# Performance work log

Measured on AMD Instinct MI355X. Metric: run time of the kernel, lower is better.

Reference implementation:

```python
import jax, jax.numpy as jnp
import numpy as np

B, R, C, D = 4, 64, 64, 512   # batch, rows, cols, hidden_size
H, DH = 4, 128                # num_heads, channels per head
S = R * C                     # flattened attention length (raster order)
NEG = -1e6                    # mask value used by coltran


def setup_inputs():
    key = jax.random.key(0)
    ks = jax.random.split(key, 7)
    def w(k, shape, s=0.02):
        return jax.random.normal(k, shape, jnp.float32) * s
    return dict(
        x=jax.random.normal(ks[0], (B, R, C, D), jnp.float32),
        wq=w(ks[1], (D, H, DH)),
        wk=w(ks[2], (D, H, DH)),
        wv=w(ks[3], (D, H, DH)),
        wo=w(ks[4], (H, DH, D)),
        # relative_attention_bias_i: [num_heads, 2*length] per axis
        # (zero-init in the original; randomized here so the bias path is exercised)
        rel_row=w(ks[5], (H, 2 * R)),
        rel_col=w(ks[6], (H, 2 * C)),
    )


def _axis_bias(w, L):
    """att_utils.relative_attn_bias: [H, 2L] -> [H, Lq, Lk], b[h,q,k] = w[h, L-1 + k - q]."""
    pos = jnp.arange(L)
    idx = (L - 1) + pos[None, :] - pos[:, None]  # [Lq, Lk] in [0, 2L-2]
    return w[:, idx]


def reference(x, wq, wk, wv, wo, rel_row, rel_col):
    # q/k/v projections: contract channel axis into [H, DH]
    q = jnp.einsum('brcd,dhe->brche', x, wq) * (DH ** -0.5)
    k = jnp.einsum('brcd,dhe->brche', x, wk)
    v = jnp.einsum('brcd,dhe->brche', x, wv)
    q = q.reshape(B, S, H, DH)
    k = k.reshape(B, S, H, DH)
    v = v.reshape(B, S, H, DH)

    # factorized N-D relative attention bias -> [H, S, S]
    brow = _axis_bias(rel_row, R)  # [H, R, R]
    bcol = _axis_bias(rel_col, C)  # [H, C, C]
    bias = (brow[:, :, None, :, None] + bcol[:, None, :, None, :]).reshape(H, S, S)

    # 'future' mask in raster order: disallow k > q
    mask = jnp.triu(jnp.full((S, S), NEG, dtype=jnp.float32), 1)

    logits = jnp.einsum('bqhe,bkhe->bhqk', q, k) + bias[None] + mask[None, None]
    p = jax.nn.softmax(logits, axis=-1)
    o = jnp.einsum('bhqk,bkhe->bqhe', p, v)       # weighted sum over keys
    out = jnp.einsum('bqhe,hed->bqd', o, wo)      # final projection, contract_axes=2
    return out.reshape(B, R, C, D)
```

## Files before the change

### kernel.cpp

```cpp
#include <hip/hip_runtime.h>
#include <cstdint>

typedef unsigned short u16;
typedef __attribute__((ext_vector_type(8))) short short8;
typedef __attribute__((ext_vector_type(4))) short short4v;
typedef __attribute__((ext_vector_type(4))) float f32x4;
typedef __attribute__((ext_vector_type(4))) unsigned short u16x4;
typedef __attribute__((ext_vector_type(2))) float f32x2;
typedef __attribute__((ext_vector_type(2))) __bf16 bf16x2;


#if defined(__has_builtin)
#if __has_builtin(__builtin_amdgcn_mfma_f32_16x16x16bf16_1k)
#define HAVE_MFMA16 1
#endif
#endif

__device__ __forceinline__ uint32_t pk2(float a, float b) {
  f32x2 t;
  t[0] = a;
  t[1] = b;
  bf16x2 h = __builtin_convertvector(t, bf16x2);
  return __builtin_bit_cast(uint32_t, h);
}

__device__ __forceinline__ u16 f2b(float f) {
  return __builtin_bit_cast(u16, (__bf16)f);
}

__device__ __forceinline__ uint2 pkbf16x4(f32x4 v, float s) {
  uint2 r;
  r.x = pk2(v[0] * s, v[1] * s);
  r.y = pk2(v[2] * s, v[3] * s);
  return r;
}

__device__ __forceinline__ void dma16(const u16* g, u16* l) {
  __builtin_amdgcn_global_load_lds(
      (const __attribute__((address_space(1))) unsigned int*)(uintptr_t)g,
      (__attribute__((address_space(3))) unsigned int*)(uintptr_t)l, 16, 0, 0);
}

#define LDS_FENCE() asm volatile("s_waitcnt lgkmcnt(0)" ::: "memory")

__global__ __launch_bounds__(256) void xcast(const float* __restrict__ x,
                                             u16* __restrict__ xb) {
  const size_t i = (size_t)(blockIdx.x * 256 + threadIdx.x) * 8;
  const float4 a = *(const float4*)(x + i);
  const float4 b = *(const float4*)(x + i + 4);
  uint4 o;
  o.x = pk2(a.x, a.y);
  o.y = pk2(a.z, a.w);
  o.z = pk2(b.x, b.y);
  o.w = pk2(b.z, b.w);
  *(uint4*)(xb + i) = o;
}

__global__ __launch_bounds__(256) void transpose_all(const float* __restrict__ wq,
                                                     const float* __restrict__ wk,
                                                     const float* __restrict__ wv,
                                                     const float* __restrict__ wo,
                                                     u16* __restrict__ wT,
                                                     u16* __restrict__ woT) {
  __shared__ __align__(16) u16 T[64][68];
  const int mtx = blockIdx.y;
  const float* src = (mtx == 0) ? wq : (mtx == 1) ? wk : (mtx == 2) ? wv : wo;
  u16* dst = (mtx < 3) ? (wT + (size_t)mtx * 262144) : woT;
  const int tr = blockIdx.x >> 3, tc = blockIdx.x & 7;
  const int tid = threadIdx.x;
#pragma unroll
  for (int p = 0; p < 4; ++p) {
    int i = p * 256 + tid;
    int row = i >> 4, c4 = i & 15;
    float4 v = *(const float4*)(src + (size_t)(tr * 64 + row) * 512 + tc * 64 + c4 * 4);
    T[c4 * 4 + 0][row] = f2b(v.x);
    T[c4 * 4 + 1][row] = f2b(v.y);
    T[c4 * 4 + 2][row] = f2b(v.z);
    T[c4 * 4 + 3][row] = f2b(v.w);
  }
  __syncthreads();
#pragma unroll
  for (int p = 0; p < 4; ++p) {
    int i = p * 256 + tid;
    int row = i >> 4, c4 = i & 15;
    *(u16x4*)(dst + (size_t)(tc * 64 + row) * 512 + tr * 64 + c4 * 4) =
        *(const u16x4*)&T[row][c4 * 4];
  }
}

__global__ __launch_bounds__(512, 2) void qkv_gemm(const u16* __restrict__ xb,
                                                   const u16* __restrict__ wT_all,
                                                   u16* __restrict__ qbuf,
                                                   u16* __restrict__ kbuf,
                                                   u16* __restrict__ vtbuf) {
  __shared__ __align__(16) u16 smem[128 * 72 + 256 * 72];
  u16* As = smem;
  u16* Bs = smem + 128 * 72;
  const int tid = threadIdx.x;
  const int wave = tid >> 6, lane = tid & 63, quad = lane >> 4, l16 = lane & 15;
  const int wm = wave >> 2, wn = wave & 3;
  const int m0 = blockIdx.x * 128;
  const int which = blockIdx.y >> 1;
  const int n0 = (blockIdx.y & 1) * 256;
  const u16* wTb = wT_all + (size_t)which * 262144 + (size_t)n0 * 512;

  f32x4 acc[4][4];
  const f32x4 fz = {0.f, 0.f, 0.f, 0.f};
#pragma unroll
  for (int i = 0; i < 4; ++i)
#pragma unroll
    for (int j = 0; j < 4; ++j) acc[i][j] = fz;

  for (int k0 = 0; k0 < 512; k0 += 64) {
#pragma unroll
    for (int p = 0; p < 2; ++p) {
      int i = p * 512 + tid, row = i >> 3, c8 = i & 7;
      uint4 v = *(const uint4*)(xb + (size_t)(m0 + row) * 512 + k0 + c8 * 8);
      *(uint4*)&As[row * 72 + c8 * 8] = v;
    }
#pragma unroll
    for (int p = 0; p < 4; ++p) {
      int i = p * 512 + tid, row = i >> 3, c8 = i & 7;
      uint4 v = *(const uint4*)(wTb + (size_t)row * 512 + k0 + c8 * 8);
      *(uint4*)&Bs[row * 72 + c8 * 8] = v;
    }
    __syncthreads();
#pragma unroll
    for (int ks = 0; ks < 2; ++ks) {
      short8 xf[4], wf[4];
#pragma unroll
      for (int mt = 0; mt < 4; ++mt)
        xf[mt] = *(const short8*)&As[(wm * 64 + mt * 16 + l16) * 72 + ks * 32 + quad * 8];
#pragma unroll
      for (int nt = 0; nt < 4; ++nt)
        wf[nt] = *(const short8*)&Bs[(wn * 64 + nt * 16 + l16) * 72 + ks * 32 + quad * 8];
      if (which < 2) {
#pragma unroll
        for (int mt = 0; mt < 4; ++mt)
#pragma unroll
          for (int nt = 0; nt < 4; ++nt)
            acc[mt][nt] = __builtin_amdgcn_mfma_f32_16x16x32_bf16(wf[nt], xf[mt],
                                                                  acc[mt][nt], 0, 0, 0);
      } else {
#pragma unroll
        for (int mt = 0; mt < 4; ++mt)
#pragma unroll
          for (int nt = 0; nt < 4; ++nt)
            acc[mt][nt] = __builtin_amdgcn_mfma_f32_16x16x32_bf16(xf[mt], wf[nt],
                                                                  acc[mt][nt], 0, 0, 0);
      }
    }
    __syncthreads();
  }
  u16* sw = smem + wave * 3072;
  const int dhg0 = n0 + wn * 64;
  const int h = dhg0 >> 7, dhh0 = dhg0 & 127;
  const int bq = m0 >> 12;
  const int bh = bq * 4 + h;
  const int sl0 = (m0 & 4095) + wm * 64;

  if (which < 2) {
    const float scl = (which == 0) ? 0.08838834764831845f : 1.0f;
    u16* dst = (which == 0) ? qbuf : kbuf;
#pragma unroll
    for (int mt = 0; mt < 4; ++mt) {
      LDS_FENCE();
#pragma unroll
      for (int nt = 0; nt < 4; ++nt)
        *(uint2*)&sw[l16 * 68 + nt * 16 + quad * 4] = pkbf16x4(acc[mt][nt], scl);
      LDS_FENCE();
#pragma unroll
      for (int p = 0; p < 2; ++p) {
        const int sr = p * 8 + (lane >> 3), dl = (lane & 7) * 8;
        uint4 v = *(const uint4*)&sw[sr * 68 + dl];
        const int sl = sl0 + mt * 16 + sr;
        *(uint4*)(dst + ((size_t)(bh * 4096 + sl)) * 128 + dhh0 + dl) = v;
      }
    }
  } else {
#pragma unroll
    for (int p2 = 0; p2 < 2; ++p2) {
      LDS_FENCE();
#pragma unroll
      for (int m2 = 0; m2 < 2; ++m2) {
        const int mt = p2 * 2 + m2;
#pragma unroll
        for (int nt = 0; nt < 4; ++nt)
          *(uint2*)&sw[(nt * 16 + l16) * 36 + m2 * 16 + quad * 4] =
              pkbf16x4(acc[mt][nt], 1.0f);
      }
      LDS_FENCE();
#pragma unroll
      for (int j = 0; j < 4; ++j) {
        const int dl = j * 16 + (lane >> 2), so = (lane & 3) * 8;
        uint4 v = *(const uint4*)&sw[dl * 36 + so];
        const int sl = sl0 + p2 * 32 + so;
        *(uint4*)(vtbuf + ((size_t)(bh * 128 + dhh0 + dl)) * 4096 + sl) = v;
      }
    }
  }
}

__global__ __launch_bounds__(256, 4) void attn(const u16* __restrict__ qbuf,
                                               const u16* __restrict__ kbuf,
                                               const u16* __restrict__ vtbuf,
                                               const float* __restrict__ rel_row,
                                               const float* __restrict__ rel_col,
                                               u16* __restrict__ obuf,
                                               float* __restrict__ opart,
                                               float* __restrict__ lpart) {
  __shared__ __align__(16) u16 KsF[64 * 128];
  __shared__ __align__(16) u16 VtF[128 * 64];
#ifndef HAVE_MFMA16
  __shared__ __align__(16) u16 Plds[4][16][72];
#endif
  __shared__ float rcol[128];
  __shared__ float rrow[128];

  const int tid = threadIdx.x;
  const int wave = tid >> 6, lane = tid & 63, quad = lane >> 4, l16 = lane & 15;
  const int jid = blockIdx.x;
  const int bh = jid & 15, p = (jid >> 4) & 31, half = jid >> 9;
  const int b = bh >> 2, h = bh & 3;

  const float LOG2E = 1.4426950408889634f;
  if (tid < 128) rcol[tid] = rel_col[h * 128 + tid] * LOG2E;
  else rrow[tid - 128] = rel_row[h * 128 + (tid - 128)] * LOG2E;

  const int q_loc = wave * 16 + l16;
  const int qc = q_loc;

  __syncthreads();

  float rc2[4][4];
#pragma unroll
  for (int nt = 0; nt < 4; ++nt)
#pragma unroll
    for (int r = 0; r < 4; ++r)
      rc2[nt][r] = rcol[63 + nt * 16 + quad * 4 + r - qc];

  const f32x4 fz = {0.f, 0.f, 0.f, 0.f};
  const u16* kbase = kbuf + (size_t)bh * 4096 * 128;
  const u16* vbase = vtbuf + (size_t)bh * 128 * 4096;
  const int krow = tid >> 4, kcs = ((tid & 15) ^ (krow & 7)) * 8;
  const int vrow = tid >> 3, vcs = ((tid & 7) ^ (vrow & 7)) * 8;
  u16* kdst = KsF + wave * 512;
  u16* vdst = VtF + wave * 512;

  auto run_row = [&](int r, int ktb, int kte, bool direct) {
    const u16* qrow = qbuf + ((size_t)bh * 4096 + r * 64 + q_loc) * 128;
    short8 qf[4];
#pragma unroll
    for (int ks = 0; ks < 4; ++ks) qf[ks] = *(const short8*)(qrow + ks * 32 + quad * 8);
    f32x4 oacc[8];
#pragma unroll
    for (int i = 0; i < 8; ++i) oacc[i] = fz;
    float l_run = 0.0f;

    for (int kt = ktb; kt < kte; ++kt) {
      __syncthreads();
      {
        const u16* ksrc = kbase + (size_t)kt * 8192;
        const u16* vsrc = vbase + kt * 64;
#pragma unroll
        for (int j = 0; j < 4; ++j)
          dma16(ksrc + (size_t)(j * 16 + krow) * 128 + kcs, kdst + j * 2048);
#pragma unroll
        for (int j = 0; j < 4; ++j)
          dma16(vsrc + (size_t)(j * 32 + vrow) * 4096 + vcs, vdst + j * 2048);
      }
      __syncthreads();

      f32x4 sacc[4];
#pragma unroll
      for (int nt = 0; nt < 4; ++nt) sacc[nt] = fz;
      __builtin_amdgcn_s_setprio(1);
#pragma unroll
      for (int ks = 0; ks < 4; ++ks)
#pragma unroll
        for (int nt = 0; nt < 4; ++nt) {
          short8 kf = *(const short8*)&KsF[(nt * 16 + l16) * 128 +
                                           ((ks * 32 + quad * 8) ^ ((l16 & 7) * 8))];
          sacc[nt] = __builtin_amdgcn_mfma_f32_16x16x32_bf16(kf, qf[ks], sacc[nt], 0, 0, 0);
        }
      __builtin_amdgcn_s_setprio(0);

      const float browl = rrow[63 + kt - r];
      const bool diag = (kt == r);
      uint2 pd[4];
#pragma unroll
      for (int nt = 0; nt < 4; ++nt) {
        f32x4 pv;
#pragma unroll
        for (int rr = 0; rr < 4; ++rr) {
          const int kc2 = nt * 16 + quad * 4 + rr;
          float pe = __builtin_amdgcn_exp2f(fmaf(sacc[nt][rr], LOG2E, rc2[nt][rr] + browl));
          if (diag && kc2 > qc) pe = 0.0f;
          l_run += pe;
          pv[rr] = pe;
        }
        pd[nt].x = pk2(pv[0], pv[1]);
        pd[nt].y = pk2(pv[2], pv[3]);
      }

#ifdef HAVE_MFMA16
      __builtin_amdgcn_s_setprio(1);
#pragma unroll
      for (int nt = 0; nt < 4; ++nt) {
        short4v pf = __builtin_bit_cast(short4v, pd[nt]);
#pragma unroll
        for (int mt = 0; mt < 8; ++mt) {
          short4v vf = *(const short4v*)&VtF[(mt * 16 + l16) * 64 +
                                             ((nt * 16 + quad * 4) ^ ((l16 & 7) * 8))];
          oacc[mt] = __builtin_amdgcn_mfma_f32_16x16x16bf16_1k(vf, pf, oacc[mt], 0, 0, 0);
        }
      }
      __builtin_amdgcn_s_setprio(0);
#else
#pragma unroll
      for (int nt = 0; nt < 4; ++nt)
        *(uint2*)&Plds[wave][l16][nt * 16 + quad * 4] = pd[nt];
#pragma unroll
      for (int ks2 = 0; ks2 < 2; ++ks2) {
        short8 pf = *(const short8*)&Plds[wave][l16][ks2 * 32 + quad * 8];
#pragma unroll
        for (int mt = 0; mt < 8; ++mt) {
          short8 vf = *(const short8*)&VtF[(mt * 16 + l16) * 64 +
                                           ((ks2 * 32 + quad * 8) ^ ((l16 & 7) * 8))];
          oacc[mt] = __builtin_amdgcn_mfma_f32_16x16x32_bf16(vf, pf, oacc[mt], 0, 0, 0);
        }
      }
#endif
    }

    l_run += __shfl_xor(l_run, 16);
    l_run += __shfl_xor(l_run, 32);
    if (direct) {
      const float inv_l = 1.0f / l_run;
      u16* orow = obuf + ((size_t)b * 4096 + r * 64 + q_loc) * 512 + h * 128;
#pragma unroll
      for (int mt = 0; mt < 8; ++mt)
        *(uint2*)(orow + mt * 16 + quad * 4) = pkbf16x4(oacc[mt], inv_l);
    } else {
      const size_t qi = (size_t)((half * 16 + bh) * 32 + (r - 32)) * 64 + q_loc;
      float* od = opart + qi * 128;
#pragma unroll
      for (int mt = 0; mt < 8; ++mt)
        *(f32x4*)(od + mt * 16 + quad * 4) = oacc[mt];
      if (quad == 0) lpart[qi] = l_run;
    }
  };

  if (half == 0) {
    run_row(p, 0, p + 1, true);
    run_row(63 - p, 0, 32 - p, false);
  } else {
    run_row(63 - p, 32 - p, 64 - p, false);
  }
}

__global__ __launch_bounds__(256) void onorm(const float* __restrict__ opart,
                                             const float* __restrict__ lpart,
                                             u16* __restrict__ obuf) {
  const int gi = blockIdx.x * 256 + threadIdx.x;
  const int d8 = (gi & 15) * 8;
  const int qi = gi >> 4;
  const int q = qi & 63, rr = (qi >> 6) & 31, bh = qi >> 11;
  const float inv = 1.0f / (lpart[qi] + lpart[32768 + qi]);
  const float* s0 = opart + (size_t)qi * 128 + d8;
  const float* s1 = s0 + 4194304;
  f32x4 a0 = *(const f32x4*)s0;
  f32x4 b0 = *(const f32x4*)(s0 + 4);
  f32x4 a1 = *(const f32x4*)s1;
  f32x4 b1 = *(const f32x4*)(s1 + 4);
  f32x4 sa = a0 + a1, sb = b0 + b1;
  uint4 o;
  o.x = pk2(sa[0] * inv, sa[1] * inv);
  o.y = pk2(sa[2] * inv, sa[3] * inv);
  o.z = pk2(sb[0] * inv, sb[1] * inv);
  o.w = pk2(sb[2] * inv, sb[3] * inv);
  const int b = bh >> 2, h = bh & 3;
  const int q_glob = (32 + rr) * 64 + q;
  *(uint4*)(obuf + ((size_t)b * 4096 + q_glob) * 512 + h * 128 + d8) = o;
}

__global__ __launch_bounds__(512, 2) void out_gemm(const u16* __restrict__ obuf,
                                                   const u16* __restrict__ woT,
                                                   float* __restrict__ out) {
  __shared__ __align__(16) u16 smem[128 * 72 + 256 * 72];
  u16* As = smem;
  u16* Bs = smem + 128 * 72;
  const int tid = threadIdx.x;
  const int wave = tid >> 6, lane = tid & 63, quad = lane >> 4, l16 = lane & 15;
  const int wm = wave >> 2, wn = wave & 3;
  const int m0 = blockIdx.x * 128;
  const int n0 = blockIdx.y * 256;

  f32x4 acc[4][4];
  const f32x4 fz = {0.f, 0.f, 0.f, 0.f};
#pragma unroll
  for (int i = 0; i < 4; ++i)
#pragma unroll
    for (int j = 0; j < 4; ++j) acc[i][j] = fz;

  for (int k0 = 0; k0 < 512; k0 += 64) {
#pragma unroll
    for (int p = 0; p < 2; ++p) {
      int i = p * 512 + tid, row = i >> 3, c8 = i & 7;
      uint4 v = *(const uint4*)(obuf + (size_t)(m0 + row) * 512 + k0 + c8 * 8);
      *(uint4*)&As[row * 72 + c8 * 8] = v;
    }
#pragma unroll
    for (int p = 0; p < 4; ++p) {
      int i = p * 512 + tid, row = i >> 3, c8 = i & 7;
      uint4 v = *(const uint4*)(woT + (size_t)(n0 + row) * 512 + k0 + c8 * 8);
      *(uint4*)&Bs[row * 72 + c8 * 8] = v;
    }
    __syncthreads();
#pragma unroll
    for (int ks = 0; ks < 2; ++ks) {
      short8 of[4], wf[4];
#pragma unroll
      for (int mt = 0; mt < 4; ++mt)
        of[mt] = *(const short8*)&As[(wm * 64 + mt * 16 + l16) * 72 + ks * 32 + quad * 8];
#pragma unroll
      for (int nt = 0; nt < 4; ++nt)
        wf[nt] = *(const short8*)&Bs[(wn * 64 + nt * 16 + l16) * 72 + ks * 32 + quad * 8];
#pragma unroll
      for (int mt = 0; mt < 4; ++mt)
#pragma unroll
        for (int nt = 0; nt < 4; ++nt)
          acc[mt][nt] = __builtin_amdgcn_mfma_f32_16x16x32_bf16(wf[nt], of[mt],
                                                                acc[mt][nt], 0, 0, 0);
    }
    __syncthreads();
  }

  float* swf = (float*)smem + wave * 1536;
#pragma unroll
  for (int mt = 0; mt < 4; ++mt) {
    LDS_FENCE();
#pragma unroll
    for (int nt = 0; nt < 4; ++nt)
      *(f32x4*)&swf[l16 * 68 + nt * 16 + quad * 4] = acc[mt][nt];
    LDS_FENCE();
#pragma unroll
    for (int p = 0; p < 4; ++p) {
      const int sr = p * 4 + (lane >> 4), dl = l16 * 4;
      float4 v = *(const float4*)&swf[sr * 68 + dl];
      const int s = m0 + wm * 64 + mt * 16 + sr;
      *(float4*)(out + (size_t)s * 512 + n0 + wn * 64 + dl) = v;
    }
  }
}

extern "C" void kernel_launch(void* const* d_in, const int* in_sizes, int n_in,
                              void* d_out, int out_size, void* d_ws, size_t ws_size,
                              hipStream_t stream) {
  const float* x       = (const float*)d_in[0];
  const float* wq      = (const float*)d_in[1];
  const float* wk      = (const float*)d_in[2];
  const float* wv      = (const float*)d_in[3];
  const float* wo      = (const float*)d_in[4];
  const float* rel_row = (const float*)d_in[5];
  const float* rel_col = (const float*)d_in[6];
  float* out = (float*)d_out;

  char* ws = (char*)d_ws;
  u16* wT    = (u16*)(ws);
  u16* woT   = (u16*)(ws + 1572864);
  u16* qbuf  = (u16*)(ws + 2097152);
  u16* kbuf  = (u16*)(ws + 2097152 + 16777216);
  u16* vtbuf = (u16*)(ws + 2097152 + 2 * 16777216);
  u16* obuf  = (u16*)(ws + 2097152 + 3 * 16777216);
  float* opart = (float*)(ws + 2097152 + 4 * 16777216);
  float* lpart = (float*)(ws + 2097152 + 6 * 16777216);
  u16* xb    = obuf;

  xcast<<<4096, 256, 0, stream>>>(x, xb);
  transpose_all<<<dim3(64, 4), 256, 0, stream>>>(wq, wk, wv, wo, wT, woT);
  qkv_gemm<<<dim3(128, 6), 512, 0, stream>>>(xb, wT, qbuf, kbuf, vtbuf);
  attn<<<1024, 256, 0, stream>>>(qbuf, kbuf, vtbuf, rel_row, rel_col, obuf, opart, lpart);
  onorm<<<2048, 256, 0, stream>>>(opart, lpart, obuf);
  out_gemm<<<dim3(128, 2), 512, 0, stream>>>(obuf, woT, out);
}
```

Measured before the change: 277.6 us.

## Process two 16-query groups per wave in attention with 128-thread blocks

The attention kernel now uses 2 waves per block instead of 4. Each wave handles 32 query rows as two 16-row groups, so every K/V fragment loaded from LDS feeds two MFMAs. This halves LDS fragment reads per MFMA and spreads the tile DMA over fewer threads. In exchange, register pressure roughly doubles for accumulators and Q fragments, and there are fewer waves per block to hide latency, which could reduce occupancy.

After: 270.9 us. 2.4% less time.

```diff
diff --git a/kernel.cpp b/kernel.cpp
--- a/kernel.cpp
+++ b/kernel.cpp
@@ -201,7 +201,7 @@
   }
 }
 
-__global__ __launch_bounds__(256, 4) void attn(const u16* __restrict__ qbuf,
+__global__ __launch_bounds__(128, 2) void attn(const u16* __restrict__ qbuf,
                                                const u16* __restrict__ kbuf,
                                                const u16* __restrict__ vtbuf,
                                                const float* __restrict__ rel_row,
@@ -212,7 +212,7 @@
   __shared__ __align__(16) u16 KsF[64 * 128];
   __shared__ __align__(16) u16 VtF[128 * 64];
 #ifndef HAVE_MFMA16
-  __shared__ __align__(16) u16 Plds[4][16][72];
+  __shared__ __align__(16) u16 Plds[2][2][16][72];
 #endif
   __shared__ float rcol[128];
   __shared__ float rrow[128];
@@ -224,38 +224,46 @@
   const int b = bh >> 2, h = bh & 3;
 
   const float LOG2E = 1.4426950408889634f;
-  if (tid < 128) rcol[tid] = rel_col[h * 128 + tid] * LOG2E;
-  else rrow[tid - 128] = rel_row[h * 128 + (tid - 128)] * LOG2E;
-
-  const int q_loc = wave * 16 + l16;
-  const int qc = q_loc;
+  rcol[tid] = rel_col[h * 128 + tid] * LOG2E;
+  rrow[tid] = rel_row[h * 128 + tid] * LOG2E;
+
+  const int q0 = wave * 32 + l16;
 
   __syncthreads();
 
-  float rc2[4][4];
-#pragma unroll
-  for (int nt = 0; nt < 4; ++nt)
-#pragma unroll
-    for (int r = 0; r < 4; ++r)
-      rc2[nt][r] = rcol[63 + nt * 16 + quad * 4 + r - qc];
+  float rc2[2][4][4];
+#pragma unroll
+  for (int g = 0; g < 2; ++g)
+#pragma unroll
+    for (int nt = 0; nt < 4; ++nt)
+#pragma unroll
+      for (int r = 0; r < 4; ++r)
+        rc2[g][nt][r] = rcol[63 + nt * 16 + quad * 4 + r - (q0 + g * 16)];
 
   const f32x4 fz = {0.f, 0.f, 0.f, 0.f};
   const u16* kbase = kbuf + (size_t)bh * 4096 * 128;
   const u16* vbase = vtbuf + (size_t)bh * 128 * 4096;
-  const int krow = tid >> 4, kcs = ((tid & 15) ^ (krow & 7)) * 8;
-  const int vrow = tid >> 3, vcs = ((tid & 7) ^ (vrow & 7)) * 8;
+  const int krow = wave * 4 + (lane >> 4);
+  const int kcs = ((lane & 15) ^ krow) * 8;
+  const int vrow = wave * 8 + (lane >> 3);
+  const int vcs = ((lane & 7) ^ (vrow & 7)) * 8;
   u16* kdst = KsF + wave * 512;
   u16* vdst = VtF + wave * 512;
 
   auto run_row = [&](int r, int ktb, int kte, bool direct) {
-    const u16* qrow = qbuf + ((size_t)bh * 4096 + r * 64 + q_loc) * 128;
-    short8 qf[4];
-#pragma unroll
-    for (int ks = 0; ks < 4; ++ks) qf[ks] = *(const short8*)(qrow + ks * 32 + quad * 8);
-    f32x4 oacc[8];
-#pragma unroll
-    for (int i = 0; i < 8; ++i) oacc[i] = fz;
-    float l_run = 0.0f;
+    const u16* qrow0 = qbuf + ((size_t)bh * 4096 + r * 64 + q0) * 128;
+    short8 qf[2][4];
+#pragma unroll
+    for (int g = 0; g < 2; ++g)
+#pragma unroll
+      for (int ks = 0; ks < 4; ++ks)
+        qf[g][ks] = *(const short8*)(qrow0 + (size_t)g * 16 * 128 + ks * 32 + quad * 8);
+    f32x4 oacc[2][8];
+#pragma unroll
+    for (int g = 0; g < 2; ++g)
+#pragma unroll
+      for (int i = 0; i < 8; ++i) oacc[g][i] = fz;
+    float l_run[2] = {0.0f, 0.0f};
 
     for (int kt = ktb; kt < kte; ++kt) {
       __syncthreads();
@@ -263,17 +271,19 @@
         const u16* ksrc = kbase + (size_t)kt * 8192;
         const u16* vsrc = vbase + kt * 64;
 #pragma unroll
-        for (int j = 0; j < 4; ++j)
-          dma16(ksrc + (size_t)(j * 16 + krow) * 128 + kcs, kdst + j * 2048);
-#pragma unroll
-        for (int j = 0; j < 4; ++j)
-          dma16(vsrc + (size_t)(j * 32 + vrow) * 4096 + vcs, vdst + j * 2048);
+        for (int j = 0; j < 8; ++j)
+          dma16(ksrc + (size_t)(j * 8 + krow) * 128 + kcs, kdst + j * 1024);
+#pragma unroll
+        for (int j = 0; j < 8; ++j)
+          dma16(vsrc + (size_t)(j * 16 + vrow) * 4096 + vcs, vdst + j * 1024);
       }
       __syncthreads();
 
-      f32x4 sacc[4];
-#pragma unroll
-      for (int nt = 0; nt < 4; ++nt) sacc[nt] = fz;
+      f32x4 sacc[2][4];
+#pragma unroll
+      for (int g = 0; g < 2; ++g)
+#pragma unroll
+        for (int nt = 0; nt < 4; ++nt) sacc[g][nt] = fz;
       __builtin_amdgcn_s_setprio(1);
 #pragma unroll
       for (int ks = 0; ks < 4; ++ks)
@@ -281,73 +291,93 @@
         for (int nt = 0; nt < 4; ++nt) {
           short8 kf = *(const short8*)&KsF[(nt * 16 + l16) * 128 +
                                            ((ks * 32 + quad * 8) ^ ((l16 & 7) * 8))];
-          sacc[nt] = __builtin_amdgcn_mfma_f32_16x16x32_bf16(kf, qf[ks], sacc[nt], 0, 0, 0);
+          sacc[0][nt] = __builtin_amdgcn_mfma_f32_16x16x32_bf16(kf, qf[0][ks], sacc[0][nt], 0, 0, 0);
+          sacc[1][nt] = __builtin_amdgcn_mfma_f32_16x16x32_bf16(kf, qf[1][ks], sacc[1][nt], 0, 0, 0);
         }
       __builtin_amdgcn_s_setprio(0);
 
       const float browl = rrow[63 + kt - r];
       const bool diag = (kt == r);
-      uint2 pd[4];
-#pragma unroll
-      for (int nt = 0; nt < 4; ++nt) {
-        f32x4 pv;
-#pragma unroll
-        for (int rr = 0; rr < 4; ++rr) {
-          const int kc2 = nt * 16 + quad * 4 + rr;
-          float pe = __builtin_amdgcn_exp2f(fmaf(sacc[nt][rr], LOG2E, rc2[nt][rr] + browl));
-          if (diag && kc2 > qc) pe = 0.0f;
-          l_run += pe;
-          pv[rr] = pe;
+      uint2 pd[2][4];
+#pragma unroll
+      for (int g = 0; g < 2; ++g) {
+        const int qc = q0 + g * 16;
+#pragma unroll
+        for (int nt = 0; nt < 4; ++nt) {
+          f32x4 pv;
+#pragma unroll
+          for (int rr = 0; rr < 4; ++rr) {
+            const int kc2 = nt * 16 + quad * 4 + rr;
+            float pe = __builtin_amdgcn_exp2f(fmaf(sacc[g][nt][rr], LOG2E, rc2[g][nt][rr] + browl));
+            if (diag && kc2 > qc) pe = 0.0f;
+            l_run[g] += pe;
+            pv[rr] = pe;
+          }
+          pd[g][nt].x = pk2(pv[0], pv[1]);
+          pd[g][nt].y = pk2(pv[2], pv[3]);
         }
-        pd[nt].x = pk2(pv[0], pv[1]);
-        pd[nt].y = pk2(pv[2], pv[3]);
       }
 
 #ifdef HAVE_MFMA16
       __builtin_amdgcn_s_setprio(1);
 #pragma unroll
       for (int nt = 0; nt < 4; ++nt) {
-        short4v pf = __builtin_bit_cast(short4v, pd[nt]);
+        short4v pf0 = __builtin_bit_cast(short4v, pd[0][nt]);
+        short4v pf1 = __builtin_bit_cast(short4v, pd[1][nt]);
 #pragma unroll
         for (int mt = 0; mt < 8; ++mt) {
           short4v vf = *(const short4v*)&VtF[(mt * 16 + l16) * 64 +
                                              ((nt * 16 + quad * 4) ^ ((l16 & 7) * 8))];
-          oacc[mt] = __builtin_amdgcn_mfma_f32_16x16x16bf16_1k(vf, pf, oacc[mt], 0, 0, 0);
+          oacc[0][mt] = __builtin_amdgcn_mfma_f32_16x16x16bf16_1k(vf, pf0, oacc[0][mt], 0, 0, 0);
+          oacc[1][mt] = __builtin_amdgcn_mfma_f32_16x16x16bf16_1k(vf, pf1, oacc[1][mt], 0, 0, 0);
         }
       }
       __builtin_amdgcn_s_setprio(0);
 #else
 #pragma unroll
-      for (int nt = 0; nt < 4; ++nt)
-        *(uint2*)&Plds[wave][l16][nt * 16 + quad * 4] = pd[nt];
-#pragma unroll
-      for (int ks2 = 0; ks2 < 2; ++ks2) {
-        short8 pf = *(const short8*)&Plds[wave][l16][ks2 * 32 + quad * 8];
-#pragma unroll
-        for (int mt = 0; mt < 8; ++mt) {
-          short8 vf = *(const short8*)&VtF[(mt * 16 + l16) * 64 +
-                                           ((ks2 * 32 + quad * 8) ^ ((l16 & 7) * 8))];
-          oacc[mt] = __builtin_amdgcn_mfma_f32_16x16x32_bf16(vf, pf, oacc[mt], 0, 0, 0);
+      for (int g = 0; g < 2; ++g)
+#pragma unroll
+        for (int nt = 0; nt < 4; ++nt)
+          *(uint2*)&Plds[wave][g][l16][nt * 16 + quad * 4] = pd[g][nt];
+#pragma unroll
+      for (int g = 0; g < 2; ++g)
+#pragma unroll
+        for (int ks2 = 0; ks2 < 2; ++ks2) {
+          short8 pf = *(const short8*)&Plds[wave][g][l16][ks2 * 32 + quad * 8];
+#pragma unroll
+          for (int mt = 0; mt < 8; ++mt) {
+            short8 vf = *(const short8*)&VtF[(mt * 16 + l16) * 64 +
+                                             ((ks2 * 32 + quad * 8) ^ ((l16 & 7) * 8))];
+            oacc[g][mt] = __builtin_amdgcn_mfma_f32_16x16x32_bf16(vf, pf, oacc[g][mt], 0, 0, 0);
+          }
         }
-      }
 #endif
     }
 
-    l_run += __shfl_xor(l_run, 16);
-    l_run += __shfl_xor(l_run, 32);
+#pragma unroll
+    for (int g = 0; g < 2; ++g) {
+      l_run[g] += __shfl_xor(l_run[g], 16);
+      l_run[g] += __shfl_xor(l_run[g], 32);
+    }
     if (direct) {
-      const float inv_l = 1.0f / l_run;
-      u16* orow = obuf + ((size_t)b * 4096 + r * 64 + q_loc) * 512 + h * 128;
-#pragma unroll
-      for (int mt = 0; mt < 8; ++mt)
-        *(uint2*)(orow + mt * 16 + quad * 4) = pkbf16x4(oacc[mt], inv_l);
+#pragma unroll
+      for (int g = 0; g < 2; ++g) {
+        const float inv_l = 1.0f / l_run[g];
+        u16* orow = obuf + ((size_t)b * 4096 + r * 64 + q0 + g * 16) * 512 + h * 128;
+#pragma unroll
+        for (int mt = 0; mt < 8; ++mt)
+          *(uint2*)(orow + mt * 16 + quad * 4) = pkbf16x4(oacc[g][mt], inv_l);
+      }
     } else {
-      const size_t qi = (size_t)((half * 16 + bh) * 32 + (r - 32)) * 64 + q_loc;
-      float* od = opart + qi * 128;
-#pragma unroll
-      for (int mt = 0; mt < 8; ++mt)
-        *(f32x4*)(od + mt * 16 + quad * 4) = oacc[mt];
-      if (quad == 0) lpart[qi] = l_run;
+#pragma unroll
+      for (int g = 0; g < 2; ++g) {
+        const size_t qi = (size_t)((half * 16 + bh) * 32 + (r - 32)) * 64 + q0 + g * 16;
+        float* od = opart + qi * 128;
+#pragma unroll
+        for (int mt = 0; mt < 8; ++mt)
+          *(f32x4*)(od + mt * 16 + quad * 4) = oacc[g][mt];
+        if (quad == 0) lpart[qi] = l_run[g];
+      }
     }
   };
 
@@ -480,7 +510,7 @@
   xcast<<<4096, 256, 0, stream>>>(x, xb);
   transpose_all<<<dim3(64, 4), 256, 0, stream>>>(wq, wk, wv, wo, wT, woT);
   qkv_gemm<<<dim3(128, 6), 512, 0, stream>>>(xb, wT, qbuf, kbuf, vtbuf);
-  attn<<<1024, 256, 0, stream>>>(qbuf, kbuf, vtbuf, rel_row, rel_col, obuf, opart, lpart);
+  attn<<<1024, 128, 0, stream>>>(qbuf, kbuf, vtbuf, rel_row, rel_col, obuf, opart, lpart);
   onorm<<<2048, 256, 0, stream>>>(opart, lpart, obuf);
   out_gemm<<<dim3(128, 2), 512, 0, stream>>>(obuf, woT, out);
 }
```
